# Kernel optimization log

Hardware: AMD Instinct MI355X
Metric: run time of the kernel (lower is better)

Reference implementation:

```python
import jax, jax.numpy as jnp
import numpy as np

B, T, I, H, O = 8192, 180, 7, 64, 16

def setup_inputs() -> dict:
    key = jax.random.key(0)
    ks = jax.random.split(key, 8)
    s_ih = 1.0 / np.sqrt(H)
    x = jax.random.normal(ks[0], (B, T, I), dtype=jnp.float32)
    # PyTorch nn.LSTM param layout: [4H, in] with gate order i, f, g, o
    W_ih = jax.random.uniform(ks[1], (4 * H, I), jnp.float32, -s_ih, s_ih)
    W_hh = jax.random.uniform(ks[2], (4 * H, H), jnp.float32, -s_ih, s_ih)
    b_ih = jax.random.uniform(ks[3], (4 * H,), jnp.float32, -s_ih, s_ih)
    b_hh = jax.random.uniform(ks[4], (4 * H,), jnp.float32, -s_ih, s_ih)
    W_fc = jax.random.uniform(ks[5], (O, H), jnp.float32, -s_ih, s_ih)
    b_fc = jax.random.uniform(ks[6], (O,), jnp.float32, -s_ih, s_ih)
    return {"x": x, "W_ih": W_ih, "W_hh": W_hh, "b_ih": b_ih,
            "b_hh": b_hh, "W_fc": W_fc, "b_fc": b_fc}

def reference(x, W_ih, W_hh, b_ih, b_hh, W_fc, b_fc):
    x = x.reshape(-1, T, I)
    b = b_ih + b_hh
    # precompute input projections for all timesteps: [T, B, 4H]
    xg = jnp.einsum('bti,gi->tbg', x, W_ih) + b

    def step(carry, xg_t):
        h, c = carry
        gates = xg_t + h @ W_hh.T  # [B, 4H]
        i_g, f_g, g_g, o_g = jnp.split(gates, 4, axis=-1)
        i_g = jax.nn.sigmoid(i_g)
        f_g = jax.nn.sigmoid(f_g)
        g_g = jnp.tanh(g_g)
        o_g = jax.nn.sigmoid(o_g)
        c = f_g * c + i_g * g_g
        h = o_g * jnp.tanh(c)
        return (h, c), None

    h0 = jnp.zeros((x.shape[0], H), dtype=x.dtype)
    c0 = jnp.zeros((x.shape[0], H), dtype=x.dtype)
    (h_last, _), _ = jax.lax.scan(step, (h0, c0), xg)
    return h_last @ W_fc.T + b_fc  # [B, O]
```

## Files before the change

kernel.cpp:

```cpp
#include <hip/hip_runtime.h>
#include <math.h>

#ifndef __has_builtin
#define __has_builtin(x) 0
#endif

#if __has_builtin(__builtin_amdgcn_rcpf)
#define FAST_RCP(x) __builtin_amdgcn_rcpf(x)
#else
#define FAST_RCP(x) (1.0f / (x))
#endif

#if __has_builtin(__builtin_amdgcn_exp2f)
#define FAST_EXP2(x) __builtin_amdgcn_exp2f(x)
#else
#define FAST_EXP2(x) exp2f(x)
#endif

__device__ __forceinline__ float fast_sigmoid(float v) {
    float e = FAST_EXP2(-1.44269504088896340736f * v);
    return FAST_RCP(1.0f + e);
}

__device__ __forceinline__ float fast_tanh(float v) {
    float e = FAST_EXP2(2.88539008177792681472f * v);
    return 1.0f - 2.0f * FAST_RCP(e + 1.0f);
}

typedef _Float16 half8 __attribute__((ext_vector_type(8)));
typedef float f32x4 __attribute__((ext_vector_type(4)));

constexpr int T_STEPS  = 180;
constexpr int I_DIM    = 7;
constexpr int HDIM     = 64;
constexpr int BT       = 16;
constexpr int BSTRIDE  = 104;

__global__ __launch_bounds__(512) void lstm_mfma_kernel(
    const float* __restrict__ x,
    const float* __restrict__ W_ih,
    const float* __restrict__ W_hh,
    const float* __restrict__ b_ih,
    const float* __restrict__ b_hh,
    const float* __restrict__ W_fc,
    const float* __restrict__ b_fc,
    float* __restrict__ out) {
    __shared__ alignas(16) _Float16 Blds[2][BT][BSTRIDE];
    __shared__ float hlds[BT][HDIM + 4];

    const int tid  = (int)threadIdx.x;
    const int w    = tid >> 6;
    const int lane = tid & 63;
    const int q    = lane >> 4;
    const int n15  = lane & 15;
    const long bbase = (long)blockIdx.x * BT;

    half8 afrag[2][3];
#pragma unroll
    for (int pt = 0; pt < 2; ++pt) {
        const int rt   = 2 * w + pt;
        const int unit = 4 * rt + (n15 >> 2);
        const int gate = n15 & 3;
        const int grow = gate * HDIM + unit;
#pragma unroll
        for (int kc = 0; kc < 3; ++kc) {
#pragma unroll
            for (int j = 0; j < 8; ++j) {
                const int k = kc * 32 + q * 8 + j;
                float v;
                if (k < I_DIM)            v = W_ih[grow * I_DIM + k];
                else if (k == I_DIM)      v = b_ih[grow] + b_hh[grow];
                else if (k < 8 + HDIM)    v = W_hh[grow * HDIM + (k - 8)];
                else                      v = 0.0f;
                afrag[pt][kc][j] = (_Float16)v;
            }
        }
    }

    for (int idx = tid; idx < 2 * BT * BSTRIDE; idx += 512) {
        const int buf = idx / (BT * BSTRIDE);
        const int rem = idx % (BT * BSTRIDE);
        const int n = rem / BSTRIDE, k = rem % BSTRIDE;
        float v = 0.0f;
        if (k == I_DIM)                 v = 1.0f;
        else if (k < I_DIM && buf == 0) v = x[(bbase + n) * (T_STEPS * I_DIM) + k];
        Blds[buf][n][k] = (_Float16)v;
    }
    __syncthreads();

    const int u0 = 8 * w + q;
    const int u1 = u0 + 4;

    const int xn = tid >> 3, xi = tid & 7;
    const bool xact = (tid < 128) && (xi < I_DIM);
    const float* xrow = x + (bbase + xn) * (T_STEPS * I_DIM);

    float c0 = 0.0f, c1 = 0.0f, h0 = 0.0f, h1 = 0.0f;

    for (int t = 0; t < T_STEPS; ++t) {
        const int cur = t & 1, nxt = cur ^ 1;

        float xpre = 0.0f;
        const bool xnow = xact && (t + 1 < T_STEPS);
        if (xnow) xpre = xrow[(t + 1) * I_DIM + xi];

        const _Float16* rb = &Blds[cur][n15][q * 8];
        const half8 bf0 = *(const half8*)(rb);
        const half8 bf1 = *(const half8*)(rb + 32);
        const half8 bf2 = *(const half8*)(rb + 64);

        f32x4 acc0 = {0.f, 0.f, 0.f, 0.f};
        f32x4 acc1 = {0.f, 0.f, 0.f, 0.f};
        acc0 = __builtin_amdgcn_mfma_f32_16x16x32_f16(afrag[0][0], bf0, acc0, 0, 0, 0);
        acc1 = __builtin_amdgcn_mfma_f32_16x16x32_f16(afrag[1][0], bf0, acc1, 0, 0, 0);
        acc0 = __builtin_amdgcn_mfma_f32_16x16x32_f16(afrag[0][1], bf1, acc0, 0, 0, 0);
        acc1 = __builtin_amdgcn_mfma_f32_16x16x32_f16(afrag[1][1], bf1, acc1, 0, 0, 0);
        acc0 = __builtin_amdgcn_mfma_f32_16x16x32_f16(afrag[0][2], bf2, acc0, 0, 0, 0);
        acc1 = __builtin_amdgcn_mfma_f32_16x16x32_f16(afrag[1][2], bf2, acc1, 0, 0, 0);

        {
            const float iv = fast_sigmoid(acc0[0]);
            const float fv = fast_sigmoid(acc0[1]);
            const float gv = fast_tanh(acc0[2]);
            const float ov = fast_sigmoid(acc0[3]);
            c0 = fv * c0 + iv * gv;
            h0 = ov * fast_tanh(c0);
        }
        {
            const float iv = fast_sigmoid(acc1[0]);
            const float fv = fast_sigmoid(acc1[1]);
            const float gv = fast_tanh(acc1[2]);
            const float ov = fast_sigmoid(acc1[3]);
            c1 = fv * c1 + iv * gv;
            h1 = ov * fast_tanh(c1);
        }

        Blds[nxt][n15][8 + u0] = (_Float16)h0;
        Blds[nxt][n15][8 + u1] = (_Float16)h1;
        if (xnow) Blds[nxt][xn][xi] = (_Float16)xpre;

        __syncthreads();
    }

    hlds[n15][u0] = h0;
    hlds[n15][u1] = h1;
    __syncthreads();
    if (tid < 256) {
        const int b = tid >> 4, j = tid & 15;
        float s = b_fc[j];
#pragma unroll 8
        for (int u = 0; u < HDIM; ++u)
            s += hlds[b][u] * W_fc[j * HDIM + u];
        out[(bbase + b) * 16 + j] = s;
    }
}

extern "C" void kernel_launch(void* const* d_in, const int* in_sizes, int n_in,
                              void* d_out, int out_size, void* d_ws, size_t ws_size,
                              hipStream_t stream) {
    const float* x    = (const float*)d_in[0];
    const float* W_ih = (const float*)d_in[1];
    const float* W_hh = (const float*)d_in[2];
    const float* b_ih = (const float*)d_in[3];
    const float* b_hh = (const float*)d_in[4];
    const float* W_fc = (const float*)d_in[5];
    const float* b_fc = (const float*)d_in[6];
    float* out = (float*)d_out;

    const int B = in_sizes[0] / (T_STEPS * I_DIM);
    const int grid = B / BT;

    lstm_mfma_kernel<<<grid, 512, 0, stream>>>(x, W_ih, W_hh, b_ih, b_hh,
                                               W_fc, b_fc, out);
}
```

Before: 230.6 us.

## Use 16 waves per block with one MFMA tile each and fold activation scales into weights

Doubles the block to 1024 threads so each wave owns a single 16-row gate tile and one LSTM cell per lane, halving the serial MFMA chain and the activation math per thread on each timestep. The exp2 scale factors for sigmoid and tanh are folded into the fp16 weights, and the gate math is rewritten to share reciprocals (i*g and o*tanh(c) each use one rcp). The cell input to tanh is clamped to avoid overflow. The cost is more waves contending at each per-timestep __syncthreads and extra rounding from pre-scaling the weights in fp16.

```diff
diff --git a/kernel.cpp b/kernel.cpp
--- a/kernel.cpp
+++ b/kernel.cpp
@@ -17,16 +17,6 @@
 #define FAST_EXP2(x) exp2f(x)
 #endif
 
-__device__ __forceinline__ float fast_sigmoid(float v) {
-    float e = FAST_EXP2(-1.44269504088896340736f * v);
-    return FAST_RCP(1.0f + e);
-}
-
-__device__ __forceinline__ float fast_tanh(float v) {
-    float e = FAST_EXP2(2.88539008177792681472f * v);
-    return 1.0f - 2.0f * FAST_RCP(e + 1.0f);
-}
-
 typedef _Float16 half8 __attribute__((ext_vector_type(8)));
 typedef float f32x4 __attribute__((ext_vector_type(4)));
 
@@ -36,7 +26,7 @@
 constexpr int BT       = 16;
 constexpr int BSTRIDE  = 104;
 
-__global__ __launch_bounds__(512) void lstm_mfma_kernel(
+__global__ __launch_bounds__(1024, 8) void lstm_mfma_kernel(
     const float* __restrict__ x,
     const float* __restrict__ W_ih,
     const float* __restrict__ W_hh,
@@ -55,13 +45,13 @@
     const int n15  = lane & 15;
     const long bbase = (long)blockIdx.x * BT;
 
-    half8 afrag[2][3];
-#pragma unroll
-    for (int pt = 0; pt < 2; ++pt) {
-        const int rt   = 2 * w + pt;
-        const int unit = 4 * rt + (n15 >> 2);
+    half8 afrag[3];
+    {
+        const int unit = 4 * w + (n15 >> 2);
         const int gate = n15 & 3;
         const int grow = gate * HDIM + unit;
+        const float scl = (gate == 2) ? 2.88539008177792681472f
+                                      : -1.44269504088896340736f;
 #pragma unroll
         for (int kc = 0; kc < 3; ++kc) {
 #pragma unroll
@@ -72,12 +62,12 @@
                 else if (k == I_DIM)      v = b_ih[grow] + b_hh[grow];
                 else if (k < 8 + HDIM)    v = W_hh[grow * HDIM + (k - 8)];
                 else                      v = 0.0f;
-                afrag[pt][kc][j] = (_Float16)v;
+                afrag[kc][j] = (_Float16)(scl * v);
             }
         }
     }
 
-    for (int idx = tid; idx < 2 * BT * BSTRIDE; idx += 512) {
+    for (int idx = tid; idx < 2 * BT * BSTRIDE; idx += 1024) {
         const int buf = idx / (BT * BSTRIDE);
         const int rem = idx % (BT * BSTRIDE);
         const int n = rem / BSTRIDE, k = rem % BSTRIDE;
@@ -88,14 +78,13 @@
     }
     __syncthreads();
 
-    const int u0 = 8 * w + q;
-    const int u1 = u0 + 4;
+    const int ucell = 4 * w + q;
 
     const int xn = tid >> 3, xi = tid & 7;
     const bool xact = (tid < 128) && (xi < I_DIM);
     const float* xrow = x + (bbase + xn) * (T_STEPS * I_DIM);
 
-    float c0 = 0.0f, c1 = 0.0f, h0 = 0.0f, h1 = 0.0f;
+    float c = 0.0f, h = 0.0f;
 
     for (int t = 0; t < T_STEPS; ++t) {
         const int cur = t & 1, nxt = cur ^ 1;
@@ -109,41 +98,32 @@
         const half8 bf1 = *(const half8*)(rb + 32);
         const half8 bf2 = *(const half8*)(rb + 64);
 
-        f32x4 acc0 = {0.f, 0.f, 0.f, 0.f};
-        f32x4 acc1 = {0.f, 0.f, 0.f, 0.f};
-        acc0 = __builtin_amdgcn_mfma_f32_16x16x32_f16(afrag[0][0], bf0, acc0, 0, 0, 0);
-        acc1 = __builtin_amdgcn_mfma_f32_16x16x32_f16(afrag[1][0], bf0, acc1, 0, 0, 0);
-        acc0 = __builtin_amdgcn_mfma_f32_16x16x32_f16(afrag[0][1], bf1, acc0, 0, 0, 0);
-        acc1 = __builtin_amdgcn_mfma_f32_16x16x32_f16(afrag[1][1], bf1, acc1, 0, 0, 0);
-        acc0 = __builtin_amdgcn_mfma_f32_16x16x32_f16(afrag[0][2], bf2, acc0, 0, 0, 0);
-        acc1 = __builtin_amdgcn_mfma_f32_16x16x32_f16(afrag[1][2], bf2, acc1, 0, 0, 0);
+        f32x4 acc = {0.f, 0.f, 0.f, 0.f};
+        acc = __builtin_amdgcn_mfma_f32_16x16x32_f16(afrag[0], bf0, acc, 0, 0, 0);
+        acc = __builtin_amdgcn_mfma_f32_16x16x32_f16(afrag[1], bf1, acc, 0, 0, 0);
+        acc = __builtin_amdgcn_mfma_f32_16x16x32_f16(afrag[2], bf2, acc, 0, 0, 0);
 
         {
-            const float iv = fast_sigmoid(acc0[0]);
-            const float fv = fast_sigmoid(acc0[1]);
-            const float gv = fast_tanh(acc0[2]);
-            const float ov = fast_sigmoid(acc0[3]);
-            c0 = fv * c0 + iv * gv;
-            h0 = ov * fast_tanh(c0);
-        }
-        {
-            const float iv = fast_sigmoid(acc1[0]);
-            const float fv = fast_sigmoid(acc1[1]);
-            const float gv = fast_tanh(acc1[2]);
-            const float ov = fast_sigmoid(acc1[3]);
-            c1 = fv * c1 + iv * gv;
-            h1 = ov * fast_tanh(c1);
+            const float A = FAST_EXP2(acc[0]);
+            const float F = FAST_EXP2(acc[1]);
+            const float E = FAST_EXP2(acc[2]);
+            const float O = FAST_EXP2(acc[3]);
+            const float ig = (E - 1.0f) * FAST_RCP((1.0f + A) * (E + 1.0f));
+            const float fv = FAST_RCP(1.0f + F);
+            c = fv * c + ig;
+            float cs = 2.88539008177792681472f * c;
+            cs = fminf(fmaxf(cs, -80.0f), 80.0f);
+            const float C = FAST_EXP2(cs);
+            h = (C - 1.0f) * FAST_RCP((1.0f + O) * (C + 1.0f));
         }
 
-        Blds[nxt][n15][8 + u0] = (_Float16)h0;
-        Blds[nxt][n15][8 + u1] = (_Float16)h1;
+        Blds[nxt][n15][8 + ucell] = (_Float16)h;
         if (xnow) Blds[nxt][xn][xi] = (_Float16)xpre;
 
         __syncthreads();
     }
 
-    hlds[n15][u0] = h0;
-    hlds[n15][u1] = h1;
+    hlds[n15][ucell] = h;
     __syncthreads();
     if (tid < 256) {
         const int b = tid >> 4, j = tid & 15;
@@ -170,6 +150,6 @@
     const int B = in_sizes[0] / (T_STEPS * I_DIM);
     const int grid = B / BT;
 
-    lstm_mfma_kernel<<<grid, 512, 0, stream>>>(x, W_ih, W_hh, b_ih, b_hh,
-                                               W_fc, b_fc, out);
+    lstm_mfma_kernel<<<grid, 1024, 0, stream>>>(x, W_ih, W_hh, b_ih, b_hh,
+                                                W_fc, b_fc, out);
 }
```

Result: no change. 228.0 us (-1.1%).
